# Kernel tuning notes

Hardware: AMD Instinct MI355X
Metric: run time of the kernel (lower is better)

## Reference

```python
import jax, jax.numpy as jnp
import numpy as np


def setup_inputs() -> dict:
    key = jax.random.key(0)
    ks = jax.random.split(key, 6)
    B, T, D, U = 32, 2048, 512, 512
    scale = 1.0 / np.sqrt(D)
    return {
        "values": jax.random.normal(ks[0], (B, T, D), dtype=jnp.float32),
        "query": jax.random.normal(ks[1], (B, D), dtype=jnp.float32),
        "W1": jax.random.normal(ks[2], (D, U), dtype=jnp.float32) * scale,
        "b1": jnp.zeros((U,), dtype=jnp.float32),
        "W2": jax.random.normal(ks[3], (D, U), dtype=jnp.float32) * scale,
        "b2": jnp.zeros((U,), dtype=jnp.float32),
        "V": jax.random.normal(ks[4], (U, 1), dtype=jnp.float32) * (1.0 / np.sqrt(U)),
        "bV": jnp.zeros((1,), dtype=jnp.float32),
    }


def reference(values, query, W1, b1, W2, b2, V, bV):
    # values: [B,T,D], query: [B,D]
    proj_v = jnp.einsum("btd,du->btu", values, W1) + b1          # [B,T,U]
    proj_q = (query @ W2 + b2)[:, None, :]                        # [B,1,U]
    score = jnp.tanh(proj_v + proj_q) @ V + bV                    # [B,T,1]
    attention_weights = jax.nn.softmax(score, axis=1)             # [B,T,1]
    context_vector = jnp.sum(attention_weights * values, axis=1)  # [B,D]
    return context_vector, attention_weights
```

## Files before the change

kernel.cpp:

```cpp
#include <hip/hip_runtime.h>
#include <math.h>


#define B_ 32
#define T_ 2048
#define D_ 512
#define U_ 512
#define M_ (B_ * T_)

typedef _Float16 half8 __attribute__((ext_vector_type(8)));
typedef float floatx4 __attribute__((ext_vector_type(4)));

__device__ __forceinline__ float fast_tanh(float x) {
  x = fminf(fmaxf(x, -20.f), 20.f);
  const float e = __expf(2.f * x);
  return 1.f - 2.f / (e + 1.f);
}

__device__ __forceinline__ void load_lds16f(const float* g, float* l) {
  __builtin_amdgcn_global_load_lds(
      (const __attribute__((address_space(1))) void*)g,
      (__attribute__((address_space(3))) void*)l, 16, 0, 0);
}

__device__ __forceinline__ void load_lds16h(const _Float16* g, _Float16* l) {
  __builtin_amdgcn_global_load_lds(
      (const __attribute__((address_space(1))) void*)g,
      (__attribute__((address_space(3))) void*)l, 16, 0, 0);
}

__global__ __launch_bounds__(256) void prep_fused(
    const float* __restrict__ W1, const float* __restrict__ query,
    const float* __restrict__ W2, const float* __restrict__ b2,
    _Float16* __restrict__ w1t, float* __restrict__ projq,
    float* __restrict__ context) {
  __shared__ float sh[64 * 65];
  const int bx = blockIdx.x;
  const int tid = threadIdx.x;
  if (bx < 64) {
    const int t = bx;
    const int k0 = (t >> 3) * 64, u0 = (t & 7) * 64;
    float(*sm)[65] = (float(*)[65])sh;
    const int lu = tid & 63;
    const int g = tid >> 6;
#pragma unroll
    for (int i = 0; i < 16; ++i) {
      const int row = g * 16 + i;
      sm[row][lu] = W1[(long)(k0 + row) * U_ + u0 + lu];
    }
    __syncthreads();
#pragma unroll
    for (int i = 0; i < 16; ++i) {
      const int row = g * 16 + i;
      w1t[(long)(u0 + row) * D_ + k0 + lu] = (_Float16)sm[lu][row];
    }
  } else {
    const int t = bx - 64;
    const int gid = t * 256 + tid;
    context[gid] = 0.f;
    const int b = t >> 1;
    const int u = (t & 1) * 256 + tid;
    for (int d = tid; d < D_; d += 256) sh[d] = query[b * D_ + d];
    __syncthreads();
    float acc = 0.f;
#pragma unroll 8
    for (int d = 0; d < D_; ++d) acc += sh[d] * W2[d * U_ + u];
    projq[b * U_ + u] = acc + b2[u];
  }
}

__global__ __launch_bounds__(512, 1) void score_fused(
    const float* __restrict__ values, const _Float16* __restrict__ w1t,
    const float* __restrict__ b1, const float* __restrict__ projq,
    const float* __restrict__ V, float* __restrict__ scores) {
  const int m0 = blockIdx.x * 128;
  const int b = blockIdx.x >> 4;
  const int tid = threadIdx.x;
  const int lane = tid & 63;
  const int w = tid >> 6;
  const int wm = (w & 1) * 64;
  const int wu = (w >> 1) * 128;
  const int ln = lane & 15;
  const int lq = lane >> 4;

  __shared__ alignas(16) float As[2][128 * 32];
  __shared__ alignas(16) _Float16 Bs[2][512 * 32];
  __shared__ float red[4][128];

  const int dr = lane >> 3;
  const int dc = (lane & 7) ^ dr;
  const float* gA[2];
#pragma unroll
  for (int j = 0; j < 2; ++j) {
    const int r = w * 16 + j * 8 + dr;
    gA[j] = values + (long)(m0 + r) * D_ + dc * 4;
  }

  const int br = lane >> 2;
  const int bc = (lane & 3) ^ (br & 3);
  const _Float16* gB[4];
#pragma unroll
  for (int i = 0; i < 4; ++i) {
    const int r = w * 64 + i * 16 + br;
    gB[i] = w1t + (long)r * D_ + bc * 8;
  }

  floatx4 acc[4][8] = {};

#pragma unroll
  for (int j = 0; j < 2; ++j)
    load_lds16f(gA[j], &As[0][(w * 16 + j * 8) * 32]);
#pragma unroll
  for (int i = 0; i < 4; ++i)
    load_lds16h(gB[i], &Bs[0][(w * 64 + i * 16) * 32]);
  __syncthreads();

  for (int t = 0; t < 16; ++t) {
    const int p = t & 1;
    if (t < 15) {
#pragma unroll
      for (int j = 0; j < 2; ++j)
        load_lds16f(gA[j] + (t + 1) * 32, &As[p ^ 1][(w * 16 + j * 8) * 32]);
#pragma unroll
      for (int i = 0; i < 4; ++i)
        load_lds16h(gB[i] + (t + 1) * 32, &Bs[p ^ 1][(w * 64 + i * 16) * 32]);
    }
    half8 bf[8];
#pragma unroll
    for (int ni = 0; ni < 8; ++ni) {
      const int r = wu + ni * 16 + ln;
      bf[ni] = *(const half8*)&Bs[p][r * 32 + ((lq ^ (ln & 3)) * 8)];
    }
    half8 af[4];
#pragma unroll
    for (int mi = 0; mi < 4; ++mi) {
      const int r = wm + mi * 16 + ln;
      const float* row = &As[p][r * 32];
      const float4 lo = *(const float4*)(row + (((2 * lq) ^ (r & 7)) * 4));
      const float4 hi = *(const float4*)(row + (((2 * lq + 1) ^ (r & 7)) * 4));
      af[mi] = half8{(_Float16)lo.x, (_Float16)lo.y, (_Float16)lo.z,
                     (_Float16)lo.w, (_Float16)hi.x, (_Float16)hi.y,
                     (_Float16)hi.z, (_Float16)hi.w};
    }
#pragma unroll
    for (int mi = 0; mi < 4; ++mi)
#pragma unroll
      for (int ni = 0; ni < 8; ++ni)
        acc[mi][ni] = __builtin_amdgcn_mfma_f32_16x16x32_f16(
            af[mi], bf[ni], acc[mi][ni], 0, 0, 0);
    __syncthreads();
  }

  float pre[8], vv[8];
#pragma unroll
  for (int ni = 0; ni < 8; ++ni) {
    const int u = wu + ni * 16 + ln;
    pre[ni] = b1[u] + projq[b * U_ + u];
    vv[ni] = V[u];
  }
#pragma unroll
  for (int mi = 0; mi < 4; ++mi) {
#pragma unroll
    for (int r = 0; r < 4; ++r) {
      float t = 0.f;
#pragma unroll
      for (int ni = 0; ni < 8; ++ni)
        t += fast_tanh(acc[mi][ni][r] + pre[ni]) * vv[ni];
      t += __shfl_xor(t, 1);
      t += __shfl_xor(t, 2);
      t += __shfl_xor(t, 4);
      t += __shfl_xor(t, 8);
      if (ln == 0) red[w >> 1][wm + mi * 16 + lq * 4 + r] = t;
    }
  }
  __syncthreads();
  if (tid < 128)
    scores[m0 + tid] =
        red[0][tid] + red[1][tid] + red[2][tid] + red[3][tid];
}

__global__ __launch_bounds__(256) void softmax_context_kernel(
    const float* __restrict__ scores, const float* __restrict__ values,
    float* __restrict__ weights, float* __restrict__ context) {
  const int b = blockIdx.x;
  const int t0 = blockIdx.y * 64;
  const int tid = threadIdx.x;

  float v[8];
  float mx = -INFINITY;
#pragma unroll
  for (int i = 0; i < 8; ++i) {
    v[i] = scores[b * T_ + i * 256 + tid];
    mx = fmaxf(mx, v[i]);
  }
#pragma unroll
  for (int off = 32; off > 0; off >>= 1) mx = fmaxf(mx, __shfl_down(mx, off));
  __shared__ float sm[4], ss[4];
  if ((tid & 63) == 0) sm[tid >> 6] = mx;
  __syncthreads();
  mx = fmaxf(fmaxf(sm[0], sm[1]), fmaxf(sm[2], sm[3]));
  float sum = 0.f;
#pragma unroll
  for (int i = 0; i < 8; ++i) sum += __expf(v[i] - mx);
#pragma unroll
  for (int off = 32; off > 0; off >>= 1) sum += __shfl_down(sum, off);
  if ((tid & 63) == 0) ss[tid >> 6] = sum;
  __syncthreads();
  const float inv = 1.f / (ss[0] + ss[1] + ss[2] + ss[3]);

  __shared__ float wsh[64];
  if (tid < 64) {
    const float ww = __expf(scores[b * T_ + t0 + tid] - mx) * inv;
    wsh[tid] = ww;
    weights[b * T_ + t0 + tid] = ww;
  }
  __syncthreads();

  const int g = tid >> 7;
  const int dx = tid & 127;
  __shared__ float4 part[128];
  float4 acc = make_float4(0.f, 0.f, 0.f, 0.f);
  const float4* vp = (const float4*)(values + (long)(b * T_ + t0 + g) * D_) + dx;
#pragma unroll 4
  for (int t = 0; t < 32; ++t) {
    const float4 x = vp[(long)(2 * t) * (D_ / 4)];
    const float ww = wsh[2 * t + g];
    acc.x += ww * x.x; acc.y += ww * x.y; acc.z += ww * x.z; acc.w += ww * x.w;
  }
  if (g == 0) part[dx] = acc;
  __syncthreads();
  if (g == 1) {
    const float4 p = part[dx];
    atomicAdd(&context[b * D_ + dx * 4 + 0], acc.x + p.x);
    atomicAdd(&context[b * D_ + dx * 4 + 1], acc.y + p.y);
    atomicAdd(&context[b * D_ + dx * 4 + 2], acc.z + p.z);
    atomicAdd(&context[b * D_ + dx * 4 + 3], acc.w + p.w);
  }
}

extern "C" void kernel_launch(void* const* d_in, const int* in_sizes, int n_in,
                              void* d_out, int out_size, void* d_ws, size_t ws_size,
                              hipStream_t stream) {
  const float* values = (const float*)d_in[0];
  const float* query = (const float*)d_in[1];
  const float* W1 = (const float*)d_in[2];
  const float* b1 = (const float*)d_in[3];
  const float* W2 = (const float*)d_in[4];
  const float* b2 = (const float*)d_in[5];
  const float* V = (const float*)d_in[6];

  float* out = (float*)d_out;
  float* context = out;
  float* weights = out + B_ * D_;
  float* projq = (float*)d_ws;
  float* scores = projq + B_ * U_;
  _Float16* w1t = (_Float16*)((char*)d_ws + 65536 + 262144);

  prep_fused<<<128, 256, 0, stream>>>(W1, query, W2, b2, w1t, projq, context);
  score_fused<<<M_ / 128, 512, 0, stream>>>(values, w1t, b1, projq, V, scores);
  softmax_context_kernel<<<dim3(B_, T_ / 64), 256, 0, stream>>>(
      scores, values, weights, context);
}
```

Baseline: 298.4 us.

## Deepen A-tile prefetch to four stages with manual vmcnt waits and split barriers

The single-barrier double-buffered loop in the score GEMM becomes a manually scheduled pipeline. The values tile (A) is prefetched two steps ahead in a 4-slot LDS ring, W1t (B) one step ahead. Raw s_waitcnt vmcnt counts and two s_barriers per step replace __syncthreads, so fragment reads finish before the MFMAs start and the next loads overlap compute. The B-tile LDS swizzle also changes to a row-pair based XOR to cut bank conflicts. This doubles A-tile LDS use, and the hand-counted vmcnt values must match the number of outstanding loads exactly or reads will race.

```diff
diff --git a/kernel.cpp b/kernel.cpp
--- a/kernel.cpp
+++ b/kernel.cpp
@@ -83,7 +83,7 @@
   const int ln = lane & 15;
   const int lq = lane >> 4;
 
-  __shared__ alignas(16) float As[2][128 * 32];
+  __shared__ alignas(16) float As[4][128 * 32];
   __shared__ alignas(16) _Float16 Bs[2][512 * 32];
   __shared__ float red[4][128];
 
@@ -97,7 +97,7 @@
   }
 
   const int br = lane >> 2;
-  const int bc = (lane & 3) ^ (br & 3);
+  const int bc = (lane & 3) ^ ((lane >> 3) & 3);
   const _Float16* gB[4];
 #pragma unroll
   for (int i = 0; i < 4; ++i) {
@@ -107,49 +107,67 @@
 
   floatx4 acc[4][8] = {};
 
-#pragma unroll
-  for (int j = 0; j < 2; ++j)
-    load_lds16f(gA[j], &As[0][(w * 16 + j * 8) * 32]);
-#pragma unroll
-  for (int i = 0; i < 4; ++i)
-    load_lds16h(gB[i], &Bs[0][(w * 64 + i * 16) * 32]);
-  __syncthreads();
-
-  for (int t = 0; t < 16; ++t) {
-    const int p = t & 1;
-    if (t < 15) {
-#pragma unroll
-      for (int j = 0; j < 2; ++j)
-        load_lds16f(gA[j] + (t + 1) * 32, &As[p ^ 1][(w * 16 + j * 8) * 32]);
-#pragma unroll
-      for (int i = 0; i < 4; ++i)
-        load_lds16h(gB[i] + (t + 1) * 32, &Bs[p ^ 1][(w * 64 + i * 16) * 32]);
-    }
+  auto issueA = [&](int T) {
+    float* dst = &As[T & 3][(w * 16) * 32];
+    const long off = (long)T * 32;
+#pragma unroll
+    for (int j = 0; j < 2; ++j)
+      load_lds16f(gA[j] + off, dst + j * 8 * 32);
+  };
+  auto issueB = [&](int T) {
+    _Float16* dst = &Bs[T & 1][(w * 64) * 32];
+    const long off = (long)T * 32;
+#pragma unroll
+    for (int i = 0; i < 4; ++i)
+      load_lds16h(gB[i] + off, dst + i * 16 * 32);
+  };
+  auto consume = [&](int t) {
+    asm volatile("s_barrier" ::: "memory");
+    const _Float16* Bp = Bs[t & 1];
+    const float* Ap = As[t & 3];
     half8 bf[8];
 #pragma unroll
     for (int ni = 0; ni < 8; ++ni) {
       const int r = wu + ni * 16 + ln;
-      bf[ni] = *(const half8*)&Bs[p][r * 32 + ((lq ^ (ln & 3)) * 8)];
+      bf[ni] = *(const half8*)&Bp[r * 32 + ((lq ^ ((r >> 1) & 3)) * 8)];
     }
     half8 af[4];
 #pragma unroll
     for (int mi = 0; mi < 4; ++mi) {
       const int r = wm + mi * 16 + ln;
-      const float* row = &As[p][r * 32];
+      const float* row = &Ap[r * 32];
       const float4 lo = *(const float4*)(row + (((2 * lq) ^ (r & 7)) * 4));
       const float4 hi = *(const float4*)(row + (((2 * lq + 1) ^ (r & 7)) * 4));
       af[mi] = half8{(_Float16)lo.x, (_Float16)lo.y, (_Float16)lo.z,
                      (_Float16)lo.w, (_Float16)hi.x, (_Float16)hi.y,
                      (_Float16)hi.z, (_Float16)hi.w};
     }
+    asm volatile("s_waitcnt lgkmcnt(0)" ::: "memory");
+    __builtin_amdgcn_sched_barrier(0);
+    asm volatile("s_barrier" ::: "memory");
 #pragma unroll
     for (int mi = 0; mi < 4; ++mi)
 #pragma unroll
       for (int ni = 0; ni < 8; ++ni)
         acc[mi][ni] = __builtin_amdgcn_mfma_f32_16x16x32_f16(
             af[mi], bf[ni], acc[mi][ni], 0, 0, 0);
-    __syncthreads();
-  }
+  };
+
+  issueA(0);
+  issueB(0);
+  issueA(1);
+
+  for (int t = 0; t < 14; ++t) {
+    issueB(t + 1);
+    issueA(t + 2);
+    asm volatile("s_waitcnt vmcnt(8)" ::: "memory");
+    consume(t);
+  }
+  issueB(15);
+  asm volatile("s_waitcnt vmcnt(6)" ::: "memory");
+  consume(14);
+  asm volatile("s_waitcnt vmcnt(0)" ::: "memory");
+  consume(15);
 
   float pre[8], vv[8];
 #pragma unroll
```

Result: slower. 305.8 us (+2.5%).

## Split score GEMM over U into smaller 64x128 tiles with atomic score reduction

Applied to the files above, without the earlier changes.

Replaces the 128-row by full-U tile per 512-thread block with 256-thread blocks computing 64 rows by a 128-wide U slice. The 4096 blocks are remapped through an XCD-aware swizzle, and partial scores are combined with atomicAdd into a scores buffer that the prep kernel now zeroes. The aim is more blocks per CU (launch bounds 256,4) and better occupancy and latency hiding. In exchange, each values tile is read four times instead of once, and atomics make the summation order nondeterministic.

```diff
diff --git a/kernel.cpp b/kernel.cpp
--- a/kernel.cpp
+++ b/kernel.cpp
@@ -33,7 +33,7 @@
     const float* __restrict__ W1, const float* __restrict__ query,
     const float* __restrict__ W2, const float* __restrict__ b2,
     _Float16* __restrict__ w1t, float* __restrict__ projq,
-    float* __restrict__ context) {
+    float* __restrict__ scores, float* __restrict__ context) {
   __shared__ float sh[64 * 65];
   const int bx = blockIdx.x;
   const int tid = threadIdx.x;
@@ -58,6 +58,7 @@
     const int t = bx - 64;
     const int gid = t * 256 + tid;
     context[gid] = 0.f;
+    ((float4*)scores)[gid] = make_float4(0.f, 0.f, 0.f, 0.f);
     const int b = t >> 1;
     const int u = (t & 1) * 256 + tid;
     for (int d = tid; d < D_; d += 256) sh[d] = query[b * D_ + d];
@@ -69,23 +70,26 @@
   }
 }
 
-__global__ __launch_bounds__(512, 1) void score_fused(
+__global__ __launch_bounds__(256, 4) void score_fused(
     const float* __restrict__ values, const _Float16* __restrict__ w1t,
     const float* __restrict__ b1, const float* __restrict__ projq,
     const float* __restrict__ V, float* __restrict__ scores) {
-  const int m0 = blockIdx.x * 128;
-  const int b = blockIdx.x >> 4;
+  const int wgid = (blockIdx.x & 7) * 512 + (blockIdx.x >> 3);
+  const int mt = wgid >> 2;
+  const int u0 = (wgid & 3) * 128;
+  const int m0 = mt * 64;
+  const int b = m0 >> 11;
   const int tid = threadIdx.x;
   const int lane = tid & 63;
   const int w = tid >> 6;
-  const int wm = (w & 1) * 64;
-  const int wu = (w >> 1) * 128;
+  const int wm = (w & 1) * 32;
+  const int wuL = (w >> 1) * 64;
   const int ln = lane & 15;
   const int lq = lane >> 4;
 
-  __shared__ alignas(16) float As[2][128 * 32];
-  __shared__ alignas(16) _Float16 Bs[2][512 * 32];
-  __shared__ float red[4][128];
+  __shared__ alignas(16) float As[2][64 * 32];
+  __shared__ alignas(16) _Float16 Bs[2][128 * 32];
+  __shared__ float red[2][64];
 
   const int dr = lane >> 3;
   const int dc = (lane & 7) ^ dr;
@@ -97,22 +101,22 @@
   }
 
   const int br = lane >> 2;
-  const int bc = (lane & 3) ^ (br & 3);
-  const _Float16* gB[4];
-#pragma unroll
-  for (int i = 0; i < 4; ++i) {
-    const int r = w * 64 + i * 16 + br;
-    gB[i] = w1t + (long)r * D_ + bc * 8;
-  }
-
-  floatx4 acc[4][8] = {};
+  const int bc = (lane & 3) ^ ((lane >> 3) & 3);
+  const _Float16* gB[2];
+#pragma unroll
+  for (int i = 0; i < 2; ++i) {
+    const int r = w * 32 + i * 16 + br;
+    gB[i] = w1t + (long)(u0 + r) * D_ + bc * 8;
+  }
+
+  floatx4 acc[2][4] = {};
 
 #pragma unroll
   for (int j = 0; j < 2; ++j)
     load_lds16f(gA[j], &As[0][(w * 16 + j * 8) * 32]);
 #pragma unroll
-  for (int i = 0; i < 4; ++i)
-    load_lds16h(gB[i], &Bs[0][(w * 64 + i * 16) * 32]);
+  for (int i = 0; i < 2; ++i)
+    load_lds16h(gB[i], &Bs[0][(w * 32 + i * 16) * 32]);
   __syncthreads();
 
   for (int t = 0; t < 16; ++t) {
@@ -122,18 +126,18 @@
       for (int j = 0; j < 2; ++j)
         load_lds16f(gA[j] + (t + 1) * 32, &As[p ^ 1][(w * 16 + j * 8) * 32]);
 #pragma unroll
-      for (int i = 0; i < 4; ++i)
-        load_lds16h(gB[i] + (t + 1) * 32, &Bs[p ^ 1][(w * 64 + i * 16) * 32]);
-    }
-    half8 bf[8];
-#pragma unroll
-    for (int ni = 0; ni < 8; ++ni) {
-      const int r = wu + ni * 16 + ln;
-      bf[ni] = *(const half8*)&Bs[p][r * 32 + ((lq ^ (ln & 3)) * 8)];
-    }
-    half8 af[4];
-#pragma unroll
-    for (int mi = 0; mi < 4; ++mi) {
+      for (int i = 0; i < 2; ++i)
+        load_lds16h(gB[i] + (t + 1) * 32, &Bs[p ^ 1][(w * 32 + i * 16) * 32]);
+    }
+    half8 bf[4];
+#pragma unroll
+    for (int ni = 0; ni < 4; ++ni) {
+      const int r = wuL + ni * 16 + ln;
+      bf[ni] = *(const half8*)&Bs[p][r * 32 + ((lq ^ ((r >> 1) & 3)) * 8)];
+    }
+    half8 af[2];
+#pragma unroll
+    for (int mi = 0; mi < 2; ++mi) {
       const int r = wm + mi * 16 + ln;
       const float* row = &As[p][r * 32];
       const float4 lo = *(const float4*)(row + (((2 * lq) ^ (r & 7)) * 4));
@@ -143,28 +147,28 @@
                      (_Float16)hi.z, (_Float16)hi.w};
     }
 #pragma unroll
-    for (int mi = 0; mi < 4; ++mi)
-#pragma unroll
-      for (int ni = 0; ni < 8; ++ni)
+    for (int mi = 0; mi < 2; ++mi)
+#pragma unroll
+      for (int ni = 0; ni < 4; ++ni)
         acc[mi][ni] = __builtin_amdgcn_mfma_f32_16x16x32_f16(
             af[mi], bf[ni], acc[mi][ni], 0, 0, 0);
     __syncthreads();
   }
 
-  float pre[8], vv[8];
-#pragma unroll
-  for (int ni = 0; ni < 8; ++ni) {
-    const int u = wu + ni * 16 + ln;
+  float pre[4], vv[4];
+#pragma unroll
+  for (int ni = 0; ni < 4; ++ni) {
+    const int u = u0 + wuL + ni * 16 + ln;
     pre[ni] = b1[u] + projq[b * U_ + u];
     vv[ni] = V[u];
   }
 #pragma unroll
-  for (int mi = 0; mi < 4; ++mi) {
+  for (int mi = 0; mi < 2; ++mi) {
 #pragma unroll
     for (int r = 0; r < 4; ++r) {
       float t = 0.f;
 #pragma unroll
-      for (int ni = 0; ni < 8; ++ni)
+      for (int ni = 0; ni < 4; ++ni)
         t += fast_tanh(acc[mi][ni][r] + pre[ni]) * vv[ni];
       t += __shfl_xor(t, 1);
       t += __shfl_xor(t, 2);
@@ -174,9 +178,7 @@
     }
   }
   __syncthreads();
-  if (tid < 128)
-    scores[m0 + tid] =
-        red[0][tid] + red[1][tid] + red[2][tid] + red[3][tid];
+  if (tid < 64) atomicAdd(scores + m0 + tid, red[0][tid] + red[1][tid]);
 }
 
 __global__ __launch_bounds__(256) void softmax_context_kernel(
@@ -256,8 +258,9 @@
   float* scores = projq + B_ * U_;
   _Float16* w1t = (_Float16*)((char*)d_ws + 65536 + 262144);
 
-  prep_fused<<<128, 256, 0, stream>>>(W1, query, W2, b2, w1t, projq, context);
-  score_fused<<<M_ / 128, 512, 0, stream>>>(values, w1t, b1, projq, V, scores);
+  prep_fused<<<128, 256, 0, stream>>>(W1, query, W2, b2, w1t, projq, scores,
+                                      context);
+  score_fused<<<4096, 256, 0, stream>>>(values, w1t, b1, projq, V, scores);
   softmax_context_kernel<<<dim3(B_, T_ / 64), 256, 0, stream>>>(
       scores, values, weights, context);
 }
```

Measured after the change: 331.3 us. 11.0% more time.
